# Performance work log

Measured on AMD Instinct MI355X. Metric: run time of the kernel, lower is better.

The kernel has to match this reference:

```python
import jax, jax.numpy as jnp
import numpy as np

EPS = 1e-5
C = 1.0
SQRT_C = 1.0
MAX_NORM = 0.95


def _log0(y):
    # log map at origin: atanh(sqrt(c)||y||) * y / (sqrt(c)||y||)
    norm = jnp.clip(jnp.linalg.norm(y, axis=-1, keepdims=True), EPS)
    arg = jnp.clip(SQRT_C * norm, None, 1.0 - EPS)
    return jnp.arctanh(arg) * y / (SQRT_C * norm)


def _exp0(v):
    # exp map at origin: tanh(sqrt(c)||v||) * v / (sqrt(c)||v||)
    norm = jnp.clip(jnp.linalg.norm(v, axis=-1, keepdims=True), EPS)
    return jnp.tanh(SQRT_C * norm) * v / (SQRT_C * norm)


def _proj(x):
    # project onto Poincare ball of radius MAX_NORM/sqrt(c)
    max_r = MAX_NORM / SQRT_C
    norm = jnp.linalg.norm(x, axis=-1, keepdims=True)
    return jnp.where(norm > max_r, x * max_r / jnp.clip(norm, EPS), x)


def _hyp_linear(x, W, b):
    # log -> euclidean linear -> exp -> project
    v = _log0(x)
    v = v @ W.T + b
    return _proj(_exp0(v))


def _hyp_graph_conv(x, src, dst, n_nodes, Wm, bm, Wu, bu):
    # 1. hyperbolic linear message transform
    h = _hyp_linear(x, Wm, bm)
    # 2. tangent-space (hyperbolic) mean aggregation over incoming edges
    t = _log0(h[src])                                   # [E, D]
    summed = jax.ops.segment_sum(t, dst, num_segments=n_nodes)
    cnt = jax.ops.segment_sum(jnp.ones((src.shape[0], 1), t.dtype), dst,
                              num_segments=n_nodes)
    agg = _proj(_exp0(summed / jnp.clip(cnt, 1.0)))
    # 3. hyperbolic linear update
    return _hyp_linear(agg, Wu, bu)


def setup_inputs() -> dict:
    key = jax.random.key(0)
    k1, k2, k3, k4 = jax.random.split(key, 4)
    N, E, D, L = 50000, 800000, 128, 2
    x = jax.random.normal(k1, (N, D), dtype=jnp.float32) * 0.01
    edge_index = jax.random.randint(k2, (2, E), 0, N, dtype=jnp.int32)
    msg_W = jax.random.normal(k3, (L, D, D), dtype=jnp.float32) * 0.05
    msg_b = jnp.zeros((L, D), dtype=jnp.float32)
    upd_W = jax.random.normal(k4, (L, D, D), dtype=jnp.float32) * 0.05
    upd_b = jnp.zeros((L, D), dtype=jnp.float32)
    return {"x": x, "edge_index": edge_index, "msg_W": msg_W, "msg_b": msg_b,
            "upd_W": upd_W, "upd_b": upd_b}


def reference(x, edge_index, msg_W, msg_b, upd_W, upd_b):
    src, dst = edge_index[0], edge_index[1]
    n_nodes = x.shape[0]
    h = x
    for l in range(msg_W.shape[0]):  # small fixed layer count
        h = _hyp_graph_conv(h, src, dst, n_nodes,
                            msg_W[l], msg_b[l], upd_W[l], upd_b[l])
    return h
```

## Files before the change

### kernel.cpp

```cpp
#include <hip/hip_runtime.h>
#include <math.h>

#define EPSF 1e-5f
#define MAXN 0.95f
#define DD 128

typedef unsigned short u16;
typedef __attribute__((ext_vector_type(8))) __bf16 bf16x8;
typedef __attribute__((ext_vector_type(4))) float f32x4;
typedef __attribute__((ext_vector_type(8))) unsigned short u16x8;
typedef __attribute__((ext_vector_type(4))) unsigned u32x4;

__device__ __forceinline__ u16 f2bf(float f) {
    unsigned u = __float_as_uint(f);
    return (u16)((u + 0x7FFFu + ((u >> 16) & 1u)) >> 16);
}
__device__ __forceinline__ float bf2f(u16 b) {
    return __uint_as_float(((unsigned)b) << 16);
}

__device__ __forceinline__ float chain_scale(float nrm, bool log_out) {
    float nc  = fmaxf(nrm, EPSF);
    float f   = tanhf(nc) / nc;
    float wn  = f * nrm;
    float p   = (wn > MAXN) ? (MAXN / fmaxf(wn, EPSF)) : 1.f;
    float s   = f * p;
    if (log_out) {
        float n2  = wn * p;
        float n2c = fmaxf(n2, EPSF);
        float arg = fminf(n2c, 1.f - EPSF);
        s *= atanhf(arg) / n2c;
    }
    return s;
}

__device__ __forceinline__ float agg_scale(const float* __restrict__ ssum,
                                           const int* __restrict__ rowptr,
                                           int rg) {
    int cnt = max(rowptr[rg + 1] - rowptr[rg], 1);
    float inv = 1.f / (float)cnt;
    return chain_scale(sqrtf(ssum[rg]) * inv, true) * inv;
}

__global__ __launch_bounds__(256)
void zero_int4(int4* __restrict__ p, int n4)
{
    int i = blockIdx.x * 256 + threadIdx.x;
    if (i < n4) p[i] = make_int4(0, 0, 0, 0);
}

__global__ __launch_bounds__(256)
void split_w(const float* __restrict__ msgW, const float* __restrict__ updW,
             u16* __restrict__ whi, u16* __restrict__ wlo, int L)
{
    int gid = blockIdx.x * 256 + threadIdx.x;
    int total = L * 2 * DD * DD;
    if (gid >= total) return;
    int mat = gid >> 14;
    int elem = gid & (DD * DD - 1);
    int l = mat >> 1, tpe = mat & 1;
    float f = (tpe ? updW : msgW)[(size_t)l * DD * DD + elem];
    u16 hb = f2bf(f);
    whi[gid] = hb;
    wlo[gid] = f2bf(f - bf2f(hb));
}

template<int LOG_OUT, int FP32_OUT, int F32_IN, int SCALE_IN>
__global__ __launch_bounds__(256)
void mfma_linear(const u16* __restrict__ vhi, const u16* __restrict__ vlo,
                 const float* __restrict__ xin,
                 const float* __restrict__ ssum, const int* __restrict__ rowptr,
                 const u16* __restrict__ whi, const u16* __restrict__ wlo,
                 const float* __restrict__ bias,
                 u16* __restrict__ ohi, float* __restrict__ ofp, int N)
{
    __shared__ float sred[4][64];
    __shared__ float sScale[64];
    __shared__ float sSin[SCALE_IN ? 64 : 1];
    __shared__ u16 sHi[FP32_OUT ? 1 : 64][136];

    const int tid  = threadIdx.x;
    const int w    = tid >> 6;
    const int lane = tid & 63;
    const int l15  = lane & 15, lk = lane >> 4;
    const int base = blockIdx.x * 64;

    if (SCALE_IN) {
        if (tid < 64) {
            int rg = base + tid;
            sSin[tid] = agg_scale(ssum, rowptr, rg < N ? rg : (N - 1));
        }
        __syncthreads();
    }

    bf16x8 wh[2][4], wl[2][4];
    #pragma unroll
    for (int nt = 0; nt < 2; ++nt) {
        const int j = w * 32 + nt * 16 + l15;
        #pragma unroll
        for (int kt = 0; kt < 4; ++kt) {
            const int off = j * DD + kt * 32 + lk * 8;
            wh[nt][kt] = *(const bf16x8*)(whi + off);
            wl[nt][kt] = *(const bf16x8*)(wlo + off);
        }
    }
    const float bv0 = bias[w * 32 + l15];
    const float bv1 = bias[w * 32 + 16 + l15];

    f32x4 acc[4][2];
    #pragma unroll
    for (int mt = 0; mt < 4; ++mt)
        #pragma unroll
        for (int nt = 0; nt < 2; ++nt)
            acc[mt][nt] = (f32x4){0.f, 0.f, 0.f, 0.f};

    #pragma unroll
    for (int mt = 0; mt < 4; ++mt) {
        int row = base + mt * 16 + l15;
        row = (row < N) ? row : (N - 1);
        bf16x8 ah[4], al[4];
        if (F32_IN) {
            const float* xr = xin + (size_t)row * DD + lk * 8;
            float fv[32];
            float ss = 0.f;
            #pragma unroll
            for (int kt = 0; kt < 4; ++kt) {
                float4 a = *(const float4*)(xr + kt * 32);
                float4 b = *(const float4*)(xr + kt * 32 + 4);
                fv[kt*8+0]=a.x; fv[kt*8+1]=a.y; fv[kt*8+2]=a.z; fv[kt*8+3]=a.w;
                fv[kt*8+4]=b.x; fv[kt*8+5]=b.y; fv[kt*8+6]=b.z; fv[kt*8+7]=b.w;
            }
            #pragma unroll
            for (int q = 0; q < 32; ++q) ss += fv[q] * fv[q];
            ss += __shfl_xor(ss, 16);
            ss += __shfl_xor(ss, 32);
            float nc = fmaxf(sqrtf(ss), EPSF);
            float sc = atanhf(fminf(nc, 1.f - EPSF)) / nc;
            #pragma unroll
            for (int kt = 0; kt < 4; ++kt) {
                u16x8 uh, ul;
                #pragma unroll
                for (int q = 0; q < 8; ++q) {
                    float t = fv[kt*8+q] * sc;
                    u16 hb = f2bf(t);
                    uh[q] = hb;
                    ul[q] = f2bf(t - bf2f(hb));
                }
                ah[kt] = *reinterpret_cast<bf16x8*>(&uh);
                al[kt] = *reinterpret_cast<bf16x8*>(&ul);
            }
        } else {
            const size_t ro = (size_t)row * DD + lk * 8;
            #pragma unroll
            for (int kt = 0; kt < 4; ++kt) {
                ah[kt] = *(const bf16x8*)(vhi + ro + kt * 32);
                al[kt] = *(const bf16x8*)(vlo + ro + kt * 32);
            }
        }
        #pragma unroll
        for (int kt = 0; kt < 4; ++kt) {
            #pragma unroll
            for (int nt = 0; nt < 2; ++nt) {
                acc[mt][nt] = __builtin_amdgcn_mfma_f32_16x16x32_bf16(
                    ah[kt], wh[nt][kt], acc[mt][nt], 0, 0, 0);
                acc[mt][nt] = __builtin_amdgcn_mfma_f32_16x16x32_bf16(
                    al[kt], wh[nt][kt], acc[mt][nt], 0, 0, 0);
                acc[mt][nt] = __builtin_amdgcn_mfma_f32_16x16x32_bf16(
                    ah[kt], wl[nt][kt], acc[mt][nt], 0, 0, 0);
            }
        }
    }

    #pragma unroll
    for (int mt = 0; mt < 4; ++mt) {
        #pragma unroll
        for (int r = 0; r < 4; ++r) {
            const float sv = SCALE_IN ? sSin[mt*16 + lk*4 + r] : 1.f;
            float y0 = acc[mt][0][r] * sv + bv0;
            float y1 = acc[mt][1][r] * sv + bv1;
            float part = y0 * y0 + y1 * y1;
            part += __shfl_xor(part, 1);
            part += __shfl_xor(part, 2);
            part += __shfl_xor(part, 4);
            part += __shfl_xor(part, 8);
            if (l15 == 0) sred[w][mt*16 + lk*4 + r] = part;
        }
    }
    __syncthreads();
    if (tid < 64) {
        float ss = sred[0][tid] + sred[1][tid] + sred[2][tid] + sred[3][tid];
        sScale[tid] = chain_scale(sqrtf(ss), LOG_OUT != 0);
    }
    __syncthreads();

    #pragma unroll
    for (int mt = 0; mt < 4; ++mt) {
        #pragma unroll
        for (int r = 0; r < 4; ++r) {
            const int rloc = mt*16 + lk*4 + r;
            const float s = sScale[rloc];
            const float sv = SCALE_IN ? sSin[rloc] : 1.f;
            #pragma unroll
            for (int nt = 0; nt < 2; ++nt) {
                float z = (acc[mt][nt][r] * sv + (nt ? bv1 : bv0)) * s;
                const int col = w*32 + nt*16 + l15;
                if (FP32_OUT) {
                    const int rg = base + rloc;
                    if (rg < N) ofp[(size_t)rg * DD + col] = z;
                } else {
                    sHi[rloc][col] = f2bf(z);
                }
            }
        }
    }
    if (!FP32_OUT) {
        __syncthreads();
        const int row = tid >> 2, qc = (tid & 3) * 32;
        const int rg = base + row;
        if (rg < N) {
            #pragma unroll
            for (int i = 0; i < 4; ++i)
                *(u16x8*)(ohi + (size_t)rg * DD + qc + i*8) =
                    *(const u16x8*)(&sHi[row][qc + i*8]);
        }
    }
}

__global__ __launch_bounds__(256)
void mfma_linear_fused(const u16* __restrict__ vhi, const u16* __restrict__ vlo,
                       const float* __restrict__ ssum, const int* __restrict__ rowptr,
                       const u16* __restrict__ wuh, const u16* __restrict__ wul,
                       const float* __restrict__ bu,
                       const u16* __restrict__ wmh, const u16* __restrict__ wml,
                       const float* __restrict__ bm,
                       u16* __restrict__ ohi, int N)
{
    __shared__ float sred[4][64];
    __shared__ float sScale[64];
    __shared__ float sSin[64];
    __shared__ u16 sHi[64][136];
    __shared__ u16 sLo[64][136];

    const int tid  = threadIdx.x;
    const int w    = tid >> 6;
    const int lane = tid & 63;
    const int l15  = lane & 15, lk = lane >> 4;
    const int base = blockIdx.x * 64;

    if (tid < 64) {
        int rg = base + tid;
        sSin[tid] = agg_scale(ssum, rowptr, rg < N ? rg : (N - 1));
    }
    __syncthreads();

    f32x4 acc[4][2];

    {
        bf16x8 wh[2][4], wl[2][4];
        #pragma unroll
        for (int nt = 0; nt < 2; ++nt) {
            const int j = w * 32 + nt * 16 + l15;
            #pragma unroll
            for (int kt = 0; kt < 4; ++kt) {
                const int off = j * DD + kt * 32 + lk * 8;
                wh[nt][kt] = *(const bf16x8*)(wuh + off);
                wl[nt][kt] = *(const bf16x8*)(wul + off);
            }
        }
        const float bv0 = bu[w * 32 + l15];
        const float bv1 = bu[w * 32 + 16 + l15];

        #pragma unroll
        for (int mt = 0; mt < 4; ++mt)
            #pragma unroll
            for (int nt = 0; nt < 2; ++nt)
                acc[mt][nt] = (f32x4){0.f, 0.f, 0.f, 0.f};

        #pragma unroll
        for (int mt = 0; mt < 4; ++mt) {
            int row = base + mt * 16 + l15;
            row = (row < N) ? row : (N - 1);
            const size_t ro = (size_t)row * DD + lk * 8;
            bf16x8 ah[4], al[4];
            #pragma unroll
            for (int kt = 0; kt < 4; ++kt) {
                ah[kt] = *(const bf16x8*)(vhi + ro + kt * 32);
                al[kt] = *(const bf16x8*)(vlo + ro + kt * 32);
            }
            #pragma unroll
            for (int kt = 0; kt < 4; ++kt) {
                #pragma unroll
                for (int nt = 0; nt < 2; ++nt) {
                    acc[mt][nt] = __builtin_amdgcn_mfma_f32_16x16x32_bf16(
                        ah[kt], wh[nt][kt], acc[mt][nt], 0, 0, 0);
                    acc[mt][nt] = __builtin_amdgcn_mfma_f32_16x16x32_bf16(
                        al[kt], wh[nt][kt], acc[mt][nt], 0, 0, 0);
                    acc[mt][nt] = __builtin_amdgcn_mfma_f32_16x16x32_bf16(
                        ah[kt], wl[nt][kt], acc[mt][nt], 0, 0, 0);
                }
            }
        }

        #pragma unroll
        for (int mt = 0; mt < 4; ++mt) {
            #pragma unroll
            for (int r = 0; r < 4; ++r) {
                const float sv = sSin[mt*16 + lk*4 + r];
                float y0 = acc[mt][0][r] * sv + bv0;
                float y1 = acc[mt][1][r] * sv + bv1;
                float part = y0 * y0 + y1 * y1;
                part += __shfl_xor(part, 1);
                part += __shfl_xor(part, 2);
                part += __shfl_xor(part, 4);
                part += __shfl_xor(part, 8);
                if (l15 == 0) sred[w][mt*16 + lk*4 + r] = part;
            }
        }
        __syncthreads();
        if (tid < 64) {
            float ss = sred[0][tid] + sred[1][tid] + sred[2][tid] + sred[3][tid];
            sScale[tid] = chain_scale(sqrtf(ss), true);
        }
        __syncthreads();
        #pragma unroll
        for (int mt = 0; mt < 4; ++mt) {
            #pragma unroll
            for (int r = 0; r < 4; ++r) {
                const int rloc = mt*16 + lk*4 + r;
                const float s = sScale[rloc];
                const float sv = sSin[rloc];
                #pragma unroll
                for (int nt = 0; nt < 2; ++nt) {
                    float z = (acc[mt][nt][r] * sv + (nt ? bv1 : bv0)) * s;
                    const int col = w*32 + nt*16 + l15;
                    u16 hb = f2bf(z);
                    sHi[rloc][col] = hb;
                    sLo[rloc][col] = f2bf(z - bf2f(hb));
                }
            }
        }
    }
    __syncthreads();

    {
        bf16x8 wh[2][4], wl[2][4];
        #pragma unroll
        for (int nt = 0; nt < 2; ++nt) {
            const int j = w * 32 + nt * 16 + l15;
            #pragma unroll
            for (int kt = 0; kt < 4; ++kt) {
                const int off = j * DD + kt * 32 + lk * 8;
                wh[nt][kt] = *(const bf16x8*)(wmh + off);
                wl[nt][kt] = *(const bf16x8*)(wml + off);
            }
        }
        const float bv0 = bm[w * 32 + l15];
        const float bv1 = bm[w * 32 + 16 + l15];

        #pragma unroll
        for (int mt = 0; mt < 4; ++mt)
            #pragma unroll
            for (int nt = 0; nt < 2; ++nt)
                acc[mt][nt] = (f32x4){0.f, 0.f, 0.f, 0.f};

        #pragma unroll
        for (int mt = 0; mt < 4; ++mt) {
            const int r16 = mt * 16 + l15;
            bf16x8 ah[4], al[4];
            #pragma unroll
            for (int kt = 0; kt < 4; ++kt) {
                ah[kt] = *(const bf16x8*)(&sHi[r16][kt * 32 + lk * 8]);
                al[kt] = *(const bf16x8*)(&sLo[r16][kt * 32 + lk * 8]);
            }
            #pragma unroll
            for (int kt = 0; kt < 4; ++kt) {
                #pragma unroll
                for (int nt = 0; nt < 2; ++nt) {
                    acc[mt][nt] = __builtin_amdgcn_mfma_f32_16x16x32_bf16(
                        ah[kt], wh[nt][kt], acc[mt][nt], 0, 0, 0);
                    acc[mt][nt] = __builtin_amdgcn_mfma_f32_16x16x32_bf16(
                        al[kt], wh[nt][kt], acc[mt][nt], 0, 0, 0);
                    acc[mt][nt] = __builtin_amdgcn_mfma_f32_16x16x32_bf16(
                        ah[kt], wl[nt][kt], acc[mt][nt], 0, 0, 0);
                }
            }
        }

        #pragma unroll
        for (int mt = 0; mt < 4; ++mt) {
            #pragma unroll
            for (int r = 0; r < 4; ++r) {
                float y0 = acc[mt][0][r] + bv0;
                float y1 = acc[mt][1][r] + bv1;
                float part = y0 * y0 + y1 * y1;
                part += __shfl_xor(part, 1);
                part += __shfl_xor(part, 2);
                part += __shfl_xor(part, 4);
                part += __shfl_xor(part, 8);
                if (l15 == 0) sred[w][mt*16 + lk*4 + r] = part;
            }
        }
        __syncthreads();
        if (tid < 64) {
            float ss = sred[0][tid] + sred[1][tid] + sred[2][tid] + sred[3][tid];
            sScale[tid] = chain_scale(sqrtf(ss), true);
        }
        __syncthreads();
        #pragma unroll
        for (int mt = 0; mt < 4; ++mt) {
            #pragma unroll
            for (int r = 0; r < 4; ++r) {
                const int rloc = mt*16 + lk*4 + r;
                const float s = sScale[rloc];
                #pragma unroll
                for (int nt = 0; nt < 2; ++nt) {
                    float z = (acc[mt][nt][r] + (nt ? bv1 : bv0)) * s;
                    sHi[rloc][w*32 + nt*16 + l15] = f2bf(z);
                }
            }
        }
        __syncthreads();
        const int row = tid >> 2, qc = (tid & 3) * 32;
        const int rg = base + row;
        if (rg < N) {
            #pragma unroll
            for (int i = 0; i < 4; ++i)
                *(u16x8*)(ohi + (size_t)rg * DD + qc + i*8) =
                    *(const u16x8*)(&sHi[row][qc + i*8]);
        }
    }
}

__global__ __launch_bounds__(256)
void degree_rank(const int* __restrict__ dst, int* __restrict__ deg,
                 int* __restrict__ rank, int E)
{
    int e4 = (blockIdx.x * 256 + threadIdx.x) * 4;
    if (e4 + 3 < E) {
        int4 d = *(const int4*)(dst + e4);
        int4 r;
        r.x = atomicAdd(&deg[d.x], 1);
        r.y = atomicAdd(&deg[d.y], 1);
        r.z = atomicAdd(&deg[d.z], 1);
        r.w = atomicAdd(&deg[d.w], 1);
        *(int4*)(rank + e4) = r;
    } else {
        for (int e = e4; e < E; ++e) rank[e] = atomicAdd(&deg[dst[e]], 1);
    }
}

__global__ __launch_bounds__(1024)
void scan_rowptr(const int* __restrict__ deg, int* __restrict__ rowptr, int N)
{
    __shared__ int wsum[16];
    const int t = threadIdx.x, wv = t >> 6, ln = t & 63;
    int carry = 0;
    const int nch = (N + 4095) / 4096;
    for (int c = 0; c < nch; ++c) {
        const int i = c * 4096 + t * 4;
        int4 d = *(const int4*)(deg + i);
        int e1 = d.x, e2 = e1 + d.y, e3 = e2 + d.z, tot = e3 + d.w;
        int sc = tot;
        #pragma unroll
        for (int off = 1; off < 64; off <<= 1) {
            int u = __shfl_up(sc, off);
            if (ln >= off) sc += u;
        }
        if (ln == 63) wsum[wv] = sc;
        __syncthreads();
        if (wv == 0 && ln < 16) {
            int s2 = wsum[ln];
            #pragma unroll
            for (int off = 1; off < 16; off <<= 1) {
                int u = __shfl_up(s2, off);
                if (ln >= off) s2 += u;
            }
            wsum[ln] = s2;
        }
        __syncthreads();
        const int off0 = carry + ((wv > 0) ? wsum[wv - 1] : 0) + (sc - tot);
        if (i + 3 < N) {
            *(int4*)(rowptr + i) = make_int4(off0, off0 + e1, off0 + e2, off0 + e3);
        } else {
            if (i     < N) rowptr[i]     = off0;
            if (i + 1 < N) rowptr[i + 1] = off0 + e1;
            if (i + 2 < N) rowptr[i + 2] = off0 + e2;
        }
        carry += wsum[15];
        __syncthreads();
    }
    if (t == 0) rowptr[N] = carry;
}

__global__ __launch_bounds__(256)
void fill_csr(const int* __restrict__ src, const int* __restrict__ dst,
              const int* __restrict__ rowptr, const int* __restrict__ rank,
              int* __restrict__ csr, int E)
{
    int e4 = (blockIdx.x * 256 + threadIdx.x) * 4;
    if (e4 + 3 < E) {
        int4 d = *(const int4*)(dst + e4);
        int4 r = *(const int4*)(rank + e4);
        int4 s = *(const int4*)(src + e4);
        csr[rowptr[d.x] + r.x] = s.x;
        csr[rowptr[d.y] + r.y] = s.y;
        csr[rowptr[d.z] + r.z] = s.z;
        csr[rowptr[d.w] + r.w] = s.w;
    } else {
        for (int e = e4; e < E; ++e) csr[rowptr[dst[e]] + rank[e]] = src[e];
    }
}

__global__ __launch_bounds__(256)
void csr_gather_sum(const u16* __restrict__ ghi, const int* __restrict__ rowptr,
                    const int* __restrict__ csr, u16* __restrict__ ohi,
                    u16* __restrict__ olo, float* __restrict__ ssum, int N)
{
    int node = blockIdx.x * 4 + (threadIdx.x >> 6);
    if (node >= N) return;
    const int lane = threadIdx.x & 63;
    const int eg = lane >> 4, l15 = lane & 15;
    const int beg = rowptr[node], end = rowptr[node + 1];

    float acc[8] = {0.f,0.f,0.f,0.f,0.f,0.f,0.f,0.f};
    for (int b = beg; b < end; b += 64) {
        const int cnt = min(end - b, 64);
        const int myidx = (lane < cnt) ? csr[b + lane] : 0;
        u32x4 vc;
        {
            const bool act = eg < cnt;
            const int s = __shfl(myidx, act ? eg : 0);
            if (act) vc = *(const u32x4*)(ghi + (size_t)s * DD + l15 * 8);
        }
        for (int j = 0; j < cnt; j += 4) {
            const int en = j + 4 + eg;
            const bool actn = en < cnt;
            const int sn = __shfl(myidx, actn ? en : 0);
            u32x4 vn;
            if (actn) vn = *(const u32x4*)(ghi + (size_t)sn * DD + l15 * 8);
            if (j + eg < cnt) {
                #pragma unroll
                for (int p = 0; p < 4; ++p) {
                    acc[2*p+0] += __uint_as_float(vc[p] << 16);
                    acc[2*p+1] += __uint_as_float(vc[p] & 0xffff0000u);
                }
            }
            vc = vn;
        }
    }
    #pragma unroll
    for (int q = 0; q < 8; ++q) {
        acc[q] += __shfl_xor(acc[q], 16);
        acc[q] += __shfl_xor(acc[q], 32);
    }
    float ss = 0.f;
    #pragma unroll
    for (int q = 0; q < 8; ++q) ss += acc[q] * acc[q];
    ss += __shfl_xor(ss, 1); ss += __shfl_xor(ss, 2);
    ss += __shfl_xor(ss, 4); ss += __shfl_xor(ss, 8);
    if (eg == 0) {
        u32x4 hw, lw;
        #pragma unroll
        for (int p = 0; p < 4; ++p) {
            u16 h0 = f2bf(acc[2*p+0]), h1 = f2bf(acc[2*p+1]);
            hw[p] = (unsigned)h0 | ((unsigned)h1 << 16);
            u16 l0 = f2bf(acc[2*p+0] - bf2f(h0));
            u16 l1 = f2bf(acc[2*p+1] - bf2f(h1));
            lw[p] = (unsigned)l0 | ((unsigned)l1 << 16);
        }
        *(u32x4*)(ohi + (size_t)node * DD + l15 * 8) = hw;
        *(u32x4*)(olo + (size_t)node * DD + l15 * 8) = lw;
        if (l15 == 0) ssum[node] = ss;
    }
}

extern "C" void kernel_launch(void* const* d_in, const int* in_sizes, int n_in,
                              void* d_out, int out_size, void* d_ws, size_t ws_size,
                              hipStream_t stream)
{
    const float* x     = (const float*)d_in[0];
    const int*   ei    = (const int*)d_in[1];
    const float* msg_W = (const float*)d_in[2];
    const float* msg_b = (const float*)d_in[3];
    const float* upd_W = (const float*)d_in[4];
    const float* upd_b = (const float*)d_in[5];

    const int N = in_sizes[0] / DD;
    const int E = in_sizes[1] / 2;
    const int L = in_sizes[2] / (DD * DD);

    const int* src = ei;
    const int* dst = ei + E;

    u16* Ahi  = (u16*)d_ws;
    u16* Alo  = Ahi + (size_t)N * DD;
    u16* WhiA = Alo + (size_t)N * DD;
    u16* WloA = WhiA + (size_t)2 * L * DD * DD;
    int* deg  = (int*)(WloA + (size_t)2 * L * DD * DD);
    const int degCap = ((N + 4095) / 4096) * 4096;
    int* rowptr = deg + degCap;
    int* csr    = rowptr + (N + 1);
    float* ssum = (float*)(csr + E);

    u16* Bhi  = (u16*)d_out;
    u16* Blo  = Bhi + (size_t)N * DD;
    int* rank = (int*)Blo;

    const int nodeBlocks  = (N + 63) / 64;
    const int aggBlocks   = (N + 3) / 4;
    const int edge4Blocks = ((E + 3) / 4 + 255) / 256;

    zero_int4<<<(degCap / 4 + 255) / 256, 256, 0, stream>>>((int4*)deg, degCap / 4);
    degree_rank<<<edge4Blocks, 256, 0, stream>>>(dst, deg, rank, E);
    scan_rowptr<<<1, 1024, 0, stream>>>(deg, rowptr, N);
    fill_csr<<<edge4Blocks, 256, 0, stream>>>(src, dst, rowptr, rank, csr, E);
    split_w<<<(2 * L * DD * DD + 255) / 256, 256, 0, stream>>>(
        msg_W, upd_W, WhiA, WloA, L);

    mfma_linear<1, 0, 1, 0><<<nodeBlocks, 256, 0, stream>>>(
        nullptr, nullptr, x, nullptr, nullptr,
        WhiA, WloA, msg_b, Bhi, nullptr, N);

    for (int l = 0; l < L; ++l) {
        const u16* wuh = WhiA + (size_t)(l * 2 + 1) * DD * DD;
        const u16* wul = WloA + (size_t)(l * 2 + 1) * DD * DD;

        csr_gather_sum<<<aggBlocks, 256, 0, stream>>>(
            Bhi, rowptr, csr, Ahi, Alo, ssum, N);

        if (l < L - 1) {
            const u16* wmh = WhiA + (size_t)((l + 1) * 2 + 0) * DD * DD;
            const u16* wml = WloA + (size_t)((l + 1) * 2 + 0) * DD * DD;
            mfma_linear_fused<<<nodeBlocks, 256, 0, stream>>>(
                Ahi, Alo, ssum, rowptr,
                wuh, wul, upd_b + (size_t)l * DD,
                wmh, wml, msg_b + (size_t)(l + 1) * DD,
                Bhi, N);
        } else {
            mfma_linear<0, 1, 0, 1><<<nodeBlocks, 256, 0, stream>>>(
                Ahi, Alo, nullptr, ssum, rowptr,
                wuh, wul, upd_b + (size_t)l * DD,
                nullptr, (float*)d_out, N);
        }
    }
}
```

Baseline: 255.1 us.

## Restructure fused linear kernel into per-16-row pipeline with swizzled fp32 LDS staging

The fused update+message linear kernel now processes its 64-row tile in four sequential 16-row slices. Each slice runs both GEMMs back to back, and weight fragments are re-read from global or cache per k-step instead of being held in registers. The intermediate is kept in fp32 in a small XOR-swizzled LDS buffer and split to hi/lo bf16 on read, replacing the large 64x136 hi/lo bf16 arrays. The aim is to cut register and LDS pressure for higher occupancy, at the cost of repeated weight loads and more barriers per block.

```diff
diff --git a/kernel.cpp b/kernel.cpp
--- a/kernel.cpp
+++ b/kernel.cpp
@@ -10,6 +10,8 @@
 typedef __attribute__((ext_vector_type(4))) float f32x4;
 typedef __attribute__((ext_vector_type(8))) unsigned short u16x8;
 typedef __attribute__((ext_vector_type(4))) unsigned u32x4;
+
+#define MFMA16 __builtin_amdgcn_mfma_f32_16x16x32_bf16
 
 __device__ __forceinline__ u16 f2bf(float f) {
     unsigned u = __float_as_uint(f);
@@ -161,12 +163,9 @@
         for (int kt = 0; kt < 4; ++kt) {
             #pragma unroll
             for (int nt = 0; nt < 2; ++nt) {
-                acc[mt][nt] = __builtin_amdgcn_mfma_f32_16x16x32_bf16(
-                    ah[kt], wh[nt][kt], acc[mt][nt], 0, 0, 0);
-                acc[mt][nt] = __builtin_amdgcn_mfma_f32_16x16x32_bf16(
-                    al[kt], wh[nt][kt], acc[mt][nt], 0, 0, 0);
-                acc[mt][nt] = __builtin_amdgcn_mfma_f32_16x16x32_bf16(
-                    ah[kt], wl[nt][kt], acc[mt][nt], 0, 0, 0);
+                acc[mt][nt] = MFMA16(ah[kt], wh[nt][kt], acc[mt][nt], 0, 0, 0);
+                acc[mt][nt] = MFMA16(al[kt], wh[nt][kt], acc[mt][nt], 0, 0, 0);
+                acc[mt][nt] = MFMA16(ah[kt], wl[nt][kt], acc[mt][nt], 0, 0, 0);
             }
         }
     }
@@ -235,11 +234,10 @@
                        const float* __restrict__ bm,
                        u16* __restrict__ ohi, int N)
 {
-    __shared__ float sred[4][64];
-    __shared__ float sScale[64];
+    __shared__ float sT[16 * 128];
+    __shared__ float sredA[4][16];
+    __shared__ float sredB[4][16];
     __shared__ float sSin[64];
-    __shared__ u16 sHi[64][136];
-    __shared__ u16 sLo[64][136];
 
     const int tid  = threadIdx.x;
     const int w    = tid >> 6;
@@ -253,181 +251,143 @@
     }
     __syncthreads();
 
-    f32x4 acc[4][2];
-
-    {
-        bf16x8 wh[2][4], wl[2][4];
-        #pragma unroll
-        for (int nt = 0; nt < 2; ++nt) {
-            const int j = w * 32 + nt * 16 + l15;
-            #pragma unroll
-            for (int kt = 0; kt < 4; ++kt) {
-                const int off = j * DD + kt * 32 + lk * 8;
-                wh[nt][kt] = *(const bf16x8*)(wuh + off);
-                wl[nt][kt] = *(const bf16x8*)(wul + off);
-            }
-        }
-        const float bv0 = bu[w * 32 + l15];
-        const float bv1 = bu[w * 32 + 16 + l15];
-
-        #pragma unroll
-        for (int mt = 0; mt < 4; ++mt)
-            #pragma unroll
-            for (int nt = 0; nt < 2; ++nt)
-                acc[mt][nt] = (f32x4){0.f, 0.f, 0.f, 0.f};
-
-        #pragma unroll
-        for (int mt = 0; mt < 4; ++mt) {
-            int row = base + mt * 16 + l15;
-            row = (row < N) ? row : (N - 1);
-            const size_t ro = (size_t)row * DD + lk * 8;
-            bf16x8 ah[4], al[4];
+    const float bu0 = bu[w * 32 + l15],      bu1 = bu[w * 32 + 16 + l15];
+    const float bm0 = bm[w * 32 + l15],      bm1 = bm[w * 32 + 16 + l15];
+    const int   colA = (w * 32 + l15) * DD + lk * 8;
+    const int   colB = (w * 32 + 16 + l15) * DD + lk * 8;
+
+    #pragma unroll 1
+    for (int mt = 0; mt < 4; ++mt) {
+        const int arow = min(base + mt * 16 + l15, N - 1);
+        const float sv_l = sSin[mt * 16 + l15];
+        bf16x8 ah[4], al[4];
+        {
+            const size_t ro = (size_t)arow * DD + lk * 8;
             #pragma unroll
             for (int kt = 0; kt < 4; ++kt) {
                 ah[kt] = *(const bf16x8*)(vhi + ro + kt * 32);
                 al[kt] = *(const bf16x8*)(vlo + ro + kt * 32);
             }
-            #pragma unroll
-            for (int kt = 0; kt < 4; ++kt) {
-                #pragma unroll
-                for (int nt = 0; nt < 2; ++nt) {
-                    acc[mt][nt] = __builtin_amdgcn_mfma_f32_16x16x32_bf16(
-                        ah[kt], wh[nt][kt], acc[mt][nt], 0, 0, 0);
-                    acc[mt][nt] = __builtin_amdgcn_mfma_f32_16x16x32_bf16(
-                        al[kt], wh[nt][kt], acc[mt][nt], 0, 0, 0);
-                    acc[mt][nt] = __builtin_amdgcn_mfma_f32_16x16x32_bf16(
-                        ah[kt], wl[nt][kt], acc[mt][nt], 0, 0, 0);
-                }
-            }
-        }
-
-        #pragma unroll
-        for (int mt = 0; mt < 4; ++mt) {
-            #pragma unroll
-            for (int r = 0; r < 4; ++r) {
-                const float sv = sSin[mt*16 + lk*4 + r];
-                float y0 = acc[mt][0][r] * sv + bv0;
-                float y1 = acc[mt][1][r] * sv + bv1;
-                float part = y0 * y0 + y1 * y1;
-                part += __shfl_xor(part, 1);
-                part += __shfl_xor(part, 2);
-                part += __shfl_xor(part, 4);
-                part += __shfl_xor(part, 8);
-                if (l15 == 0) sred[w][mt*16 + lk*4 + r] = part;
-            }
-        }
-        __syncthreads();
-        if (tid < 64) {
-            float ss = sred[0][tid] + sred[1][tid] + sred[2][tid] + sred[3][tid];
-            sScale[tid] = chain_scale(sqrtf(ss), true);
-        }
-        __syncthreads();
-        #pragma unroll
-        for (int mt = 0; mt < 4; ++mt) {
-            #pragma unroll
-            for (int r = 0; r < 4; ++r) {
-                const int rloc = mt*16 + lk*4 + r;
-                const float s = sScale[rloc];
-                const float sv = sSin[rloc];
-                #pragma unroll
-                for (int nt = 0; nt < 2; ++nt) {
-                    float z = (acc[mt][nt][r] * sv + (nt ? bv1 : bv0)) * s;
-                    const int col = w*32 + nt*16 + l15;
-                    u16 hb = f2bf(z);
-                    sHi[rloc][col] = hb;
-                    sLo[rloc][col] = f2bf(z - bf2f(hb));
-                }
-            }
-        }
-    }
-    __syncthreads();
-
-    {
-        bf16x8 wh[2][4], wl[2][4];
-        #pragma unroll
-        for (int nt = 0; nt < 2; ++nt) {
-            const int j = w * 32 + nt * 16 + l15;
-            #pragma unroll
-            for (int kt = 0; kt < 4; ++kt) {
-                const int off = j * DD + kt * 32 + lk * 8;
-                wh[nt][kt] = *(const bf16x8*)(wmh + off);
-                wl[nt][kt] = *(const bf16x8*)(wml + off);
-            }
-        }
-        const float bv0 = bm[w * 32 + l15];
-        const float bv1 = bm[w * 32 + 16 + l15];
-
-        #pragma unroll
-        for (int mt = 0; mt < 4; ++mt)
-            #pragma unroll
-            for (int nt = 0; nt < 2; ++nt)
-                acc[mt][nt] = (f32x4){0.f, 0.f, 0.f, 0.f};
-
-        #pragma unroll
-        for (int mt = 0; mt < 4; ++mt) {
-            const int r16 = mt * 16 + l15;
-            bf16x8 ah[4], al[4];
-            #pragma unroll
-            for (int kt = 0; kt < 4; ++kt) {
-                ah[kt] = *(const bf16x8*)(&sHi[r16][kt * 32 + lk * 8]);
-                al[kt] = *(const bf16x8*)(&sLo[r16][kt * 32 + lk * 8]);
-            }
-            #pragma unroll
-            for (int kt = 0; kt < 4; ++kt) {
-                #pragma unroll
-                for (int nt = 0; nt < 2; ++nt) {
-                    acc[mt][nt] = __builtin_amdgcn_mfma_f32_16x16x32_bf16(
-                        ah[kt], wh[nt][kt], acc[mt][nt], 0, 0, 0);
-                    acc[mt][nt] = __builtin_amdgcn_mfma_f32_16x16x32_bf16(
-                        al[kt], wh[nt][kt], acc[mt][nt], 0, 0, 0);
-                    acc[mt][nt] = __builtin_amdgcn_mfma_f32_16x16x32_bf16(
-                        ah[kt], wl[nt][kt], acc[mt][nt], 0, 0, 0);
-                }
-            }
-        }
-
-        #pragma unroll
-        for (int mt = 0; mt < 4; ++mt) {
-            #pragma unroll
-            for (int r = 0; r < 4; ++r) {
-                float y0 = acc[mt][0][r] + bv0;
-                float y1 = acc[mt][1][r] + bv1;
-                float part = y0 * y0 + y1 * y1;
-                part += __shfl_xor(part, 1);
-                part += __shfl_xor(part, 2);
-                part += __shfl_xor(part, 4);
-                part += __shfl_xor(part, 8);
-                if (l15 == 0) sred[w][mt*16 + lk*4 + r] = part;
-            }
-        }
-        __syncthreads();
-        if (tid < 64) {
-            float ss = sred[0][tid] + sred[1][tid] + sred[2][tid] + sred[3][tid];
-            sScale[tid] = chain_scale(sqrtf(ss), true);
-        }
-        __syncthreads();
-        #pragma unroll
-        for (int mt = 0; mt < 4; ++mt) {
-            #pragma unroll
-            for (int r = 0; r < 4; ++r) {
-                const int rloc = mt*16 + lk*4 + r;
-                const float s = sScale[rloc];
-                #pragma unroll
-                for (int nt = 0; nt < 2; ++nt) {
-                    float z = (acc[mt][nt][r] + (nt ? bv1 : bv0)) * s;
-                    sHi[rloc][w*32 + nt*16 + l15] = f2bf(z);
-                }
-            }
-        }
-        __syncthreads();
-        const int row = tid >> 2, qc = (tid & 3) * 32;
-        const int rg = base + row;
-        if (rg < N) {
-            #pragma unroll
-            for (int i = 0; i < 4; ++i)
-                *(u16x8*)(ohi + (size_t)rg * DD + qc + i*8) =
-                    *(const u16x8*)(&sHi[row][qc + i*8]);
-        }
+        }
+        f32x4 acc0 = (f32x4){0.f,0.f,0.f,0.f}, acc1 = (f32x4){0.f,0.f,0.f,0.f};
+        #pragma unroll
+        for (int kt = 0; kt < 4; ++kt) {
+            bf16x8 wh0 = *(const bf16x8*)(wuh + colA + kt * 32);
+            bf16x8 wl0 = *(const bf16x8*)(wul + colA + kt * 32);
+            bf16x8 wh1 = *(const bf16x8*)(wuh + colB + kt * 32);
+            bf16x8 wl1 = *(const bf16x8*)(wul + colB + kt * 32);
+            acc0 = MFMA16(ah[kt], wh0, acc0, 0, 0, 0);
+            acc0 = MFMA16(al[kt], wh0, acc0, 0, 0, 0);
+            acc0 = MFMA16(ah[kt], wl0, acc0, 0, 0, 0);
+            acc1 = MFMA16(ah[kt], wh1, acc1, 0, 0, 0);
+            acc1 = MFMA16(al[kt], wh1, acc1, 0, 0, 0);
+            acc1 = MFMA16(ah[kt], wl1, acc1, 0, 0, 0);
+        }
+        #pragma unroll
+        for (int r = 0; r < 4; ++r) {
+            const float sv = __shfl(sv_l, lk * 4 + r);
+            float y0 = fmaf(acc0[r], sv, bu0);
+            float y1 = fmaf(acc1[r], sv, bu1);
+            float part = y0 * y0 + y1 * y1;
+            part += __shfl_xor(part, 1); part += __shfl_xor(part, 2);
+            part += __shfl_xor(part, 4); part += __shfl_xor(part, 8);
+            if (l15 == 0) sredA[w][lk * 4 + r] = part;
+        }
+        __syncthreads();
+        float sc_l;
+        {
+            float ssr = sredA[0][l15] + sredA[1][l15] + sredA[2][l15] + sredA[3][l15];
+            sc_l = chain_scale(sqrtf(ssr), true);
+        }
+        #pragma unroll
+        for (int r = 0; r < 4; ++r) {
+            const float sv = __shfl(sv_l, lk * 4 + r);
+            const float s  = __shfl(sc_l, lk * 4 + r);
+            const int row = lk * 4 + r, key = row & 7;
+            {
+                const int col = w * 32 + l15;
+                float z = fmaf(acc0[r], sv, bu0) * s;
+                sT[row * 128 + (((col >> 2) ^ key) << 2) + (col & 3)] = z;
+            }
+            {
+                const int col = w * 32 + 16 + l15;
+                float z = fmaf(acc1[r], sv, bu1) * s;
+                sT[row * 128 + (((col >> 2) ^ key) << 2) + (col & 3)] = z;
+            }
+        }
+        __syncthreads();
+        #pragma unroll
+        for (int kt = 0; kt < 4; ++kt) {
+            const int key = l15 & 7;
+            const int c0 = kt * 8 + lk * 2;
+            float4 f0 = *(const float4*)(sT + l15 * 128 + (((c0    ) ^ key) << 2));
+            float4 f1 = *(const float4*)(sT + l15 * 128 + (((c0 + 1) ^ key) << 2));
+            float f[8] = {f0.x, f0.y, f0.z, f0.w, f1.x, f1.y, f1.z, f1.w};
+            u16x8 uh, ul;
+            #pragma unroll
+            for (int q = 0; q < 8; ++q) {
+                u16 hb = f2bf(f[q]);
+                uh[q] = hb;
+                ul[q] = f2bf(f[q] - bf2f(hb));
+            }
+            ah[kt] = *reinterpret_cast<bf16x8*>(&uh);
+            al[kt] = *reinterpret_cast<bf16x8*>(&ul);
+        }
+        acc0 = (f32x4){0.f,0.f,0.f,0.f}; acc1 = (f32x4){0.f,0.f,0.f,0.f};
+        #pragma unroll
+        for (int kt = 0; kt < 4; ++kt) {
+            bf16x8 wh0 = *(const bf16x8*)(wmh + colA + kt * 32);
+            bf16x8 wl0 = *(const bf16x8*)(wml + colA + kt * 32);
+            bf16x8 wh1 = *(const bf16x8*)(wmh + colB + kt * 32);
+            bf16x8 wl1 = *(const bf16x8*)(wml + colB + kt * 32);
+            acc0 = MFMA16(ah[kt], wh0, acc0, 0, 0, 0);
+            acc0 = MFMA16(al[kt], wh0, acc0, 0, 0, 0);
+            acc0 = MFMA16(ah[kt], wl0, acc0, 0, 0, 0);
+            acc1 = MFMA16(ah[kt], wh1, acc1, 0, 0, 0);
+            acc1 = MFMA16(al[kt], wh1, acc1, 0, 0, 0);
+            acc1 = MFMA16(ah[kt], wl1, acc1, 0, 0, 0);
+        }
+        #pragma unroll
+        for (int r = 0; r < 4; ++r) {
+            float y0 = acc0[r] + bm0;
+            float y1 = acc1[r] + bm1;
+            float part = y0 * y0 + y1 * y1;
+            part += __shfl_xor(part, 1); part += __shfl_xor(part, 2);
+            part += __shfl_xor(part, 4); part += __shfl_xor(part, 8);
+            if (l15 == 0) sredB[w][lk * 4 + r] = part;
+        }
+        __syncthreads();
+        {
+            float ssr = sredB[0][l15] + sredB[1][l15] + sredB[2][l15] + sredB[3][l15];
+            sc_l = chain_scale(sqrtf(ssr), true);
+        }
+        u16* sg = (u16*)sT;
+        #pragma unroll
+        for (int r = 0; r < 4; ++r) {
+            const float s = __shfl(sc_l, lk * 4 + r);
+            const int row = lk * 4 + r, key = (row & 7) << 3;
+            {
+                const int col = w * 32 + l15;
+                float z = (acc0[r] + bm0) * s;
+                sg[row * 128 + ((col & ~7) ^ key) + (col & 7)] = f2bf(z);
+            }
+            {
+                const int col = w * 32 + 16 + l15;
+                float z = (acc1[r] + bm1) * s;
+                sg[row * 128 + ((col & ~7) ^ key) + (col & 7)] = f2bf(z);
+            }
+        }
+        __syncthreads();
+        {
+            const int row = tid >> 4, c = tid & 15;
+            const int rg = base + mt * 16 + row;
+            const int key = (row & 7) << 3;
+            if (rg < N) {
+                u16x8 v = *(const u16x8*)(sg + row * 128 + ((c << 3) ^ key));
+                *(u16x8*)(ohi + (size_t)rg * DD + c * 8) = v;
+            }
+        }
+        __syncthreads();
     }
 }
 
```

Result: slower. 265.4 us (+4.0%).
